# Kernel tuning notes

Hardware: AMD Instinct MI355X
Metric: run time of the kernel (lower is better)

Reference implementation:

```python
import jax, jax.numpy as jnp
import numpy as np

B, T, D, H, K, TAU, L = 1024, 168, 32, 512, 8, 24, 2


def _cell(Wih, Whh, bih, bhh, x_t, h, c):
    # PyTorch LSTM gate order: i, f, g, o
    gates = x_t @ Wih.T + bih + h @ Whh.T + bhh  # [B, 4H]
    i, f, g, o = jnp.split(gates, 4, axis=-1)
    c = jax.nn.sigmoid(f) * c + jax.nn.sigmoid(i) * jnp.tanh(g)
    h = jax.nn.sigmoid(o) * jnp.tanh(c)
    return h, c


def setup_inputs() -> dict:
    key = jax.random.key(0)
    ks = jax.random.split(key, 22)
    s = 1.0 / np.sqrt(H)

    def u(k, shape):
        return jax.random.uniform(k, shape, jnp.float32, -s, s)

    inp = {"x": jax.random.normal(ks[0], (B, T, D), jnp.float32)}
    # encoder LSTM (layer0 input D, layer1 input H)
    inp["enc_Wih0"] = u(ks[1], (4 * H, D)); inp["enc_Whh0"] = u(ks[2], (4 * H, H))
    inp["enc_bih0"] = u(ks[3], (4 * H,));  inp["enc_bhh0"] = u(ks[4], (4 * H,))
    inp["enc_Wih1"] = u(ks[5], (4 * H, H)); inp["enc_Whh1"] = u(ks[6], (4 * H, H))
    inp["enc_bih1"] = u(ks[7], (4 * H,));  inp["enc_bhh1"] = u(ks[8], (4 * H,))
    # decoder LSTM (both layers input H since d_enopt == d_model)
    inp["dec_Wih0"] = u(ks[9], (4 * H, H));  inp["dec_Whh0"] = u(ks[10], (4 * H, H))
    inp["dec_bih0"] = u(ks[11], (4 * H,));   inp["dec_bhh0"] = u(ks[12], (4 * H,))
    inp["dec_Wih1"] = u(ks[13], (4 * H, H)); inp["dec_Whh1"] = u(ks[14], (4 * H, H))
    inp["dec_bih1"] = u(ks[15], (4 * H,));   inp["dec_bhh1"] = u(ks[16], (4 * H,))
    # output heads
    inp["W1"] = u(ks[17], (K, H)); inp["b1"] = u(ks[18], (K,))
    inp["W2"] = u(ks[19], (K, H)); inp["b2"] = u(ks[20], (K,))
    return inp


def reference(x, enc_Wih0, enc_Whh0, enc_bih0, enc_bhh0,
              enc_Wih1, enc_Whh1, enc_bih1, enc_bhh1,
              dec_Wih0, dec_Whh0, dec_bih0, dec_bhh0,
              dec_Wih1, dec_Whh1, dec_bih1, dec_bhh1,
              W1, b1, W2, b2):
    enc_params = [(enc_Wih0, enc_Whh0, enc_bih0, enc_bhh0),
                  (enc_Wih1, enc_Whh1, enc_bih1, enc_bhh1)]
    dec_params = [(dec_Wih0, dec_Whh0, dec_bih0, dec_bhh0),
                  (dec_Wih1, dec_Whh1, dec_bih1, dec_bhh1)]
    b = x.shape[0]
    h0 = jnp.zeros((L, b, H), x.dtype)
    c0 = jnp.zeros((L, b, H), x.dtype)

    def enc_step(carry, x_t):
        h, c = carry
        inp = x_t
        hs, cs = [], []
        for l, p in enumerate(enc_params):
            hn, cn = _cell(*p, inp, h[l], c[l])
            hs.append(hn); cs.append(cn); inp = hn
        return (jnp.stack(hs), jnp.stack(cs)), None

    (h, c), _ = jax.lax.scan(enc_step, (h0, c0), jnp.swapaxes(x, 0, 1))

    def dec_step(carry, _):
        h, c = carry
        inp = h[L - 1]  # feed top-layer hidden back as input
        hs, cs = [], []
        for l, p in enumerate(dec_params):
            hn, cn = _cell(*p, inp, h[l], c[l])
            hs.append(hn); cs.append(cn); inp = hn
        return (jnp.stack(hs), jnp.stack(cs)), inp  # top-layer output

    _, outs = jax.lax.scan(dec_step, (h, c), None, length=TAU)  # [TAU, B, H]
    out = jnp.swapaxes(outs, 0, 1)  # [B, TAU, H]
    mu = out @ W1.T + b1
    beta = 2.0
    sigma = jax.nn.softplus(beta * (out @ W2.T + b2)) / beta
    return mu, sigma
```

## Files before the change

### kernel.cpp

```cpp
#include <hip/hip_runtime.h>
#include <math.h>

typedef _Float16 f16;
typedef __attribute__((ext_vector_type(8))) _Float16 f16x8;
typedef __attribute__((ext_vector_type(4))) _Float16 f16x4;
typedef __attribute__((ext_vector_type(4))) float f32x4;

namespace {
constexpr int B_ = 1024, T_ = 168, H_ = 512, K_ = 8, TAU_ = 24, U_ = 192;
}

__device__ __forceinline__ float sig_(float x) { return 1.0f / (1.0f + expf(-x)); }

template<int AUX>
__device__ __forceinline__ void gl16(const f16* g, char* l) {
    __builtin_amdgcn_global_load_lds((const __attribute__((address_space(1))) void*)g,
                                     (__attribute__((address_space(3))) void*)l, 16, 0, AUX);
}
__device__ __forceinline__ void st_h_sc1(f16* p, f16 v) {
    unsigned int u = (unsigned int)__builtin_bit_cast(unsigned short, v);
    asm volatile("global_store_short %0, %1, off sc1" :: "v"(p), "v"(u) : "memory");
}
#define MFMA16 __builtin_amdgcn_mfma_f32_16x16x32_f16

struct PP {
    const f16 *xp, *w0p, *wsW;
    const float* bsum;
    const f16* hzero;
    f16 *h0r, *h1r;
    f16* h1dec;
    int *cnt0, *cnt1;
};

extern "C" __global__ void __launch_bounds__(256, 2)
lstm_persist(PP P)
{
    extern __shared__ char lds[];
    const int tid = threadIdx.x;
    const int id2 = (blockIdx.x & 7) * 64 + (blockIdx.x >> 3);
    const int wv  = id2 & 63;
    const int chain = wv & 1;
    const int tt  = wv >> 1;
    const int rt  = tt & 15;
    const int jt  = (id2 >> 6) * 2 + (tt >> 4);
    const int row0 = rt * 64;
    const int j0   = jt * 32;

    const int lane = tid & 63, wid = tid >> 6;
    const int l16 = lane & 15, lq = lane >> 4;
    const int wr = wid >> 1, wc = wid & 1;
    const int sr = tid >> 3, sl = tid & 7;
    const long ksw = (long)((sl ^ (sr & 7)) << 3);

    auto wgf = [&](int q) {
        const int r = sr + 32 * q;
        return (long)(((r >> 4) & 3) * H_ + j0 + ((r >> 6) << 4) + (r & 15));
    };
    const long wgr0 = wgf(0), wgr1 = wgf(1), wgr2 = wgf(2), wgr3 = wgf(3);
    const long wgH0 = wgr0 * H_ + ksw, wgH1 = wgr1 * H_ + ksw;
    const long wgH2 = wgr2 * H_ + ksw, wgH3 = wgr3 * H_ + ksw;
    const long aH0k = (long)(row0 + sr) * H_ + ksw, aH1k = aH0k + 32 * H_;

    const int swz = (l16 & 7) << 4;
    const int ab0 = (wr * 32 + l16) * 128;
    const int ab1 = ab0 + 2048;
    const int wb0 = (wc * 64 + 0 * 16 + l16) * 128, wb1 = (wc * 64 + 1 * 16 + l16) * 128;
    const int wb2 = (wc * 64 + 2 * 16 + l16) * 128, wb3 = (wc * 64 + 3 * 16 + l16) * 128;

    const size_t WM  = (size_t)2048 * 512;
    const long   NBH = (long)B_ * H_;
    bool dead = false;

    auto waitf = [&](const int* p) {
        if (tid == 0 && !dead) {
            int tries = 0;
            while (__hip_atomic_load(p, __ATOMIC_RELAXED,
                                     __HIP_MEMORY_SCOPE_AGENT) < 16) {
                __builtin_amdgcn_s_sleep(1);
                if (++tries > (1 << 16)) { dead = true; break; }
            }
        }
        __syncthreads();
    };
    auto sig1 = [&](int* p) {
        asm volatile("s_waitcnt vmcnt(0)" ::: "memory");
        __syncthreads();
        if (tid == 0)
            __hip_atomic_fetch_add(p, 1, __ATOMIC_RELAXED, __HIP_MEMORY_SCOPE_AGENT);
    };

    auto computeChunk = [&](char* lb, f32x4 (&acc)[4][2]) {
        #pragma unroll
        for (int ks = 0; ks < 2; ++ks) {
            const int kb = ((ks * 64) + lq * 16) ^ swz;
            f16x8 ah0 = *(const f16x8*)(lb + ab0 + kb);
            f16x8 ah1 = *(const f16x8*)(lb + ab1 + kb);
            f16x8 w0 = *(const f16x8*)(lb + 8192 + wb0 + kb);
            f16x8 w1 = *(const f16x8*)(lb + 8192 + wb1 + kb);
            f16x8 w2 = *(const f16x8*)(lb + 8192 + wb2 + kb);
            f16x8 w3 = *(const f16x8*)(lb + 8192 + wb3 + kb);
            acc[0][0] = MFMA16(ah0, w0, acc[0][0], 0, 0, 0);
            acc[0][1] = MFMA16(ah1, w0, acc[0][1], 0, 0, 0);
            acc[1][0] = MFMA16(ah0, w1, acc[1][0], 0, 0, 0);
            acc[1][1] = MFMA16(ah1, w1, acc[1][1], 0, 0, 0);
            acc[2][0] = MFMA16(ah0, w2, acc[2][0], 0, 0, 0);
            acc[2][1] = MFMA16(ah1, w2, acc[2][1], 0, 0, 0);
            acc[3][0] = MFMA16(ah0, w3, acc[3][0], 0, 0, 0);
            acc[3][1] = MFMA16(ah1, w3, acc[3][1], 0, 0, 0);
        }
    };

    auto epiF = [&](const float* bg, float* cst, f16* hout, f32x4 (&a)[4][2]) {
        const int j = j0 + wc * 16 + l16;
        const float bg0 = bg[j], bg1 = bg[H_ + j];
        const float bg2 = bg[2 * H_ + j], bg3 = bg[3 * H_ + j];
        #pragma unroll
        for (int m = 0; m < 2; ++m)
            #pragma unroll
            for (int r = 0; r < 4; ++r) {
                const int ci = m * 4 + r;
                const int bb = row0 + wr * 32 + m * 16 + lq * 4 + r;
                const long base = (long)bb * H_ + j;
                const float pi = a[0][m][r] + bg0;
                const float pf = a[1][m][r] + bg1;
                const float pg = a[2][m][r] + bg2;
                const float po = a[3][m][r] + bg3;
                const float cn = sig_(pf) * cst[ci] + sig_(pi) * tanhf(pg);
                const float hn = sig_(po) * tanhf(cn);
                cst[ci] = cn;
                st_h_sc1(&hout[base], (f16)hn);
            }
    };

    float cst[8];
    #pragma unroll
    for (int i = 0; i < 8; ++i) cst[i] = 0.f;

    auto runCell = [&](const f16* Ain, long lda, int ncIn, long Kw,
                       const f16* Wih, const f16* Hin, const f16* Whh,
                       const float* bg, f16* hout) {
        const long aA0 = (long)(row0 + sr) * lda + ksw;
        const long aA1 = aA0 + 32 * lda;
        const long wK0 = wgr0 * Kw + ksw, wK1 = wgr1 * Kw + ksw;
        const long wK2 = wgr2 * Kw + ksw, wK3 = wgr3 * Kw + ksw;
        const int NC = ncIn + 8;
        auto st = [&](int ci) {
            char* lb = lds + (ci % 3) * 24576;
            const bool inp = ci < ncIn;
            const long k0 = (long)(inp ? ci : ci - ncIn) << 6;
            const f16* Ap = inp ? Ain : Hin;
            const f16* Wp = inp ? Wih : Whh;
            gl16<16>(Ap + (inp ? aA0 : aH0k) + k0, lb + tid * 16);
            gl16<16>(Ap + (inp ? aA1 : aH1k) + k0, lb + 4096 + tid * 16);
            gl16<0>(Wp + (inp ? wK0 : wgH0) + k0, lb + 8192  + tid * 16);
            gl16<0>(Wp + (inp ? wK1 : wgH1) + k0, lb + 12288 + tid * 16);
            gl16<0>(Wp + (inp ? wK2 : wgH2) + k0, lb + 16384 + tid * 16);
            gl16<0>(Wp + (inp ? wK3 : wgH3) + k0, lb + 20480 + tid * 16);
        };
        f32x4 acc[4][2];
        #pragma unroll
        for (int nf = 0; nf < 4; ++nf)
            #pragma unroll
            for (int m = 0; m < 2; ++m)
                #pragma unroll
                for (int q = 0; q < 4; ++q) acc[nf][m][q] = 0.f;
        st(0); st(1); st(2);
        for (int i = 0; i < NC; ++i) {
            const int ahead = (NC - 1 - i) < 2 ? (NC - 1 - i) : 2;
            if      (ahead == 2) asm volatile("s_waitcnt vmcnt(12)" ::: "memory");
            else if (ahead == 1) asm volatile("s_waitcnt vmcnt(6)"  ::: "memory");
            else                 asm volatile("s_waitcnt vmcnt(0)"  ::: "memory");
            __builtin_amdgcn_s_barrier();
            computeChunk(lds + (i % 3) * 24576, acc);
            asm volatile("s_waitcnt lgkmcnt(0)" ::: "memory");
            __builtin_amdgcn_s_barrier();
            if (i + 3 < NC) st(i + 3);
        }
        epiF(bg, cst, hout, acc);
    };

    if (chain == 0) {
        for (int u = 0; u < U_; ++u) {
            const bool dec = (u >= T_);
            if (u > 0) waitf(P.cnt0 + (u - 1) * 16 + rt);
            if (dec)   waitf(P.cnt1 + (u - 1) * 16 + rt);
            else if (u >= 8) waitf(P.cnt1 + (u - 8) * 16 + rt);
            const f16* h0prev = (u == 0) ? P.hzero : P.h0r + (long)((u - 1) & 7) * NBH;
            f16* h0out = P.h0r + (long)(u & 7) * NBH;
            if (dec) {
                const f16* h1prev = (u <= T_) ? P.h1r + (long)((u - 1) & 7) * NBH
                                              : P.h1dec + (long)(u - 1 - T_) * NBH;
                runCell(h1prev, H_, 8, H_, P.wsW + 3 * WM, h0prev,
                        P.wsW + 4 * WM, P.bsum + 4096, h0out);
            } else {
                runCell(P.xp + (long)u * B_ * 64, 64, 1, 64, P.w0p, h0prev,
                        P.wsW, P.bsum, h0out);
            }
            sig1(P.cnt0 + u * 16 + rt);
        }
    } else {
        for (int u = 0; u < U_; ++u) {
            const bool dec = (u >= T_);
            waitf(P.cnt0 + u * 16 + rt);
            if (u > 0) waitf(P.cnt1 + (u - 1) * 16 + rt);
            const f16* h1prev = (u == 0) ? P.hzero
                              : (u <= T_ ? P.h1r + (long)((u - 1) & 7) * NBH
                                         : P.h1dec + (long)(u - 1 - T_) * NBH);
            f16* h1out = (u < T_) ? P.h1r + (long)(u & 7) * NBH
                                  : P.h1dec + (long)(u - T_) * NBH;
            runCell(P.h0r + (long)(u & 7) * NBH, H_, 8, H_,
                    dec ? P.wsW + 5 * WM : P.wsW + 1 * WM, h1prev,
                    dec ? P.wsW + 6 * WM : P.wsW + 2 * WM,
                    P.bsum + (dec ? 6144 : 2048), h1out);
            sig1(P.cnt1 + u * 16 + rt);
        }
    }
}

extern "C" __global__ void __launch_bounds__(256)
padx_kernel(const float* __restrict__ x, f16* __restrict__ xp)
{
    const int idx = blockIdx.x * 256 + threadIdx.x;
    const int t = idx >> 10, b = idx & 1023;
    const float* src = x + ((long)b * T_ + t) * 32;
    f16* dst = xp + (long)idx * 64;
    #pragma unroll
    for (int q = 0; q < 8; ++q) {
        float4 v = *(const float4*)&src[q * 4];
        *(f16x4*)&dst[q * 4] = (f16x4){(f16)v.x, (f16)v.y, (f16)v.z, (f16)v.w};
    }
    #pragma unroll
    for (int q = 8; q < 16; ++q) *(f16x4*)&dst[q * 4] = (f16x4){0, 0, 0, 0};
}

extern "C" __global__ void __launch_bounds__(256)
padw_kernel(const float* __restrict__ w, f16* __restrict__ dst)
{
    const int idx = blockIdx.x * 256 + threadIdx.x;
    const int row = idx >> 4, k4 = idx & 15;
    f16x4 hv = (f16x4){0, 0, 0, 0};
    if (k4 < 8) {
        float4 v = *(const float4*)&w[(long)row * 32 + k4 * 4];
        hv = (f16x4){(f16)v.x, (f16)v.y, (f16)v.z, (f16)v.w};
    }
    *(f16x4*)&dst[(long)row * 64 + k4 * 4] = hv;
}

extern "C" __global__ void __launch_bounds__(256)
wcvt_kernel(const float* s0, const float* s1, const float* s2, const float* s3,
            const float* s4, const float* s5, const float* s6, f16* dst)
{
    const int i = blockIdx.x * 256 + threadIdx.x;
    if (i >= 7 * 262144) return;
    const int m = i >> 18, off = i & 262143;
    const float* s = m == 0 ? s0 : m == 1 ? s1 : m == 2 ? s2 : m == 3 ? s3
                   : m == 4 ? s4 : m == 5 ? s5 : s6;
    float4 v = ((const float4*)s)[off];
    *(f16x4*)&dst[(long)m * 1048576 + (long)off * 4] =
        (f16x4){(f16)v.x, (f16)v.y, (f16)v.z, (f16)v.w};
}

extern "C" __global__ void __launch_bounds__(256)
bias_kernel(const float* a0, const float* b0, const float* a1, const float* b1,
            const float* a2, const float* b2, const float* a3, const float* b3,
            float* out)
{
    const int i = blockIdx.x * 256 + threadIdx.x;
    const int l = i >> 11, k = i & 2047;
    const float* pa = l == 0 ? a0 : l == 1 ? a1 : l == 2 ? a2 : a3;
    const float* pb = l == 0 ? b0 : l == 1 ? b1 : l == 2 ? b2 : b3;
    out[i] = pa[k] + pb[k];
}

extern "C" __global__ void __launch_bounds__(256)
zero16(uint4* p, int n)
{
    for (int i = blockIdx.x * 256 + threadIdx.x; i < n; i += gridDim.x * 256)
        p[i] = make_uint4(0, 0, 0, 0);
}

extern "C" __global__ void __launch_bounds__(256)
head_all(const f16* __restrict__ h1dec,
         const float* __restrict__ W1, const float* __restrict__ b1,
         const float* __restrict__ W2, const float* __restrict__ b2,
         float* __restrict__ out)
{
    const int blk = blockIdx.x;
    const int s = blk >> 6;
    const int idx = (blk & 63) * 256 + threadIdx.x;
    const int b = idx >> 4, rr = idx & 15, k = rr & 7, which = rr >> 3;
    const float* w  = (which ? W2 : W1) + (long)k * H_;
    const f16*   hp = h1dec + ((long)s * B_ + b) * H_;
    float sum = 0.f;
    for (int d = 0; d < H_; d += 8) {
        f16x8  hv = *(const f16x8*)&hp[d];
        float4 w0 = *(const float4*)&w[d];
        float4 w1 = *(const float4*)&w[d + 4];
        sum = fmaf((float)hv[0], w0.x, sum);
        sum = fmaf((float)hv[1], w0.y, sum);
        sum = fmaf((float)hv[2], w0.z, sum);
        sum = fmaf((float)hv[3], w0.w, sum);
        sum = fmaf((float)hv[4], w1.x, sum);
        sum = fmaf((float)hv[5], w1.y, sum);
        sum = fmaf((float)hv[6], w1.z, sum);
        sum = fmaf((float)hv[7], w1.w, sum);
    }
    const long o = ((long)b * TAU_ + s) * K_ + k;
    if (which == 0) {
        out[o] = sum + b1[k];
    } else {
        float z  = 2.0f * (sum + b2[k]);
        float sp = fmaxf(z, 0.0f) + log1pf(expf(-fabsf(z)));
        out[(long)B_ * TAU_ * K_ + o] = 0.5f * sp;
    }
}

extern "C" void kernel_launch(void* const* d_in, const int* in_sizes, int n_in,
                              void* d_out, int out_size, void* d_ws, size_t ws_size,
                              hipStream_t stream)
{
    (void)in_sizes; (void)n_in; (void)out_size; (void)ws_size;

    const float* x     = (const float*)d_in[0];
    const float* eWih0 = (const float*)d_in[1];
    const float* eWhh0 = (const float*)d_in[2];
    const float* ebih0 = (const float*)d_in[3];
    const float* ebhh0 = (const float*)d_in[4];
    const float* eWih1 = (const float*)d_in[5];
    const float* eWhh1 = (const float*)d_in[6];
    const float* ebih1 = (const float*)d_in[7];
    const float* ebhh1 = (const float*)d_in[8];
    const float* dWih0 = (const float*)d_in[9];
    const float* dWhh0 = (const float*)d_in[10];
    const float* dbih0 = (const float*)d_in[11];
    const float* dbhh0 = (const float*)d_in[12];
    const float* dWih1 = (const float*)d_in[13];
    const float* dWhh1 = (const float*)d_in[14];
    const float* dbih1 = (const float*)d_in[15];
    const float* dbhh1 = (const float*)d_in[16];
    const float* W1    = (const float*)d_in[17];
    const float* b1    = (const float*)d_in[18];
    const float* W2    = (const float*)d_in[19];
    const float* b2    = (const float*)d_in[20];
    float* out = (float*)d_out;

    (void)hipFuncSetAttribute((const void*)lstm_persist,
                              hipFuncAttributeMaxDynamicSharedMemorySize, 73728);

    char* wsp = (char*)d_ws;
    auto take = [&](size_t n) { void* p = (void*)wsp; wsp += n; return p; };

    f16* xp    = (f16*)take((size_t)T_ * B_ * 64 * 2);
    f16* w0p   = (f16*)take((size_t)2048 * 64 * 2);
    f16* wsW   = (f16*)take((size_t)7 * 2048 * 512 * 2);
    float* bsum = (float*)take((size_t)4 * 2048 * 4);
    f16* h1dec = (f16*)take((size_t)TAU_ * B_ * H_ * 2);
    f16* h0r   = (f16*)take((size_t)8 * B_ * H_ * 2);
    f16* h1r   = (f16*)take((size_t)8 * B_ * H_ * 2);

    char* zstart = wsp;
    int* cnt0  = (int*)take((size_t)U_ * 16 * 4);
    int* cnt1  = (int*)take((size_t)U_ * 16 * 4);
    f16* hzero = (f16*)take((size_t)B_ * H_ * 2);
    const size_t zeroBytes = (size_t)(wsp - zstart);

    const dim3 blk(256);

    padx_kernel<<<dim3(T_ * B_ / 256), blk, 0, stream>>>(x, xp);
    padw_kernel<<<dim3(128), blk, 0, stream>>>(eWih0, w0p);
    wcvt_kernel<<<dim3(7168), blk, 0, stream>>>(eWhh0, eWih1, eWhh1, dWih0,
                                                dWhh0, dWih1, dWhh1, wsW);
    bias_kernel<<<dim3(32), blk, 0, stream>>>(ebih0, ebhh0, ebih1, ebhh1,
                                              dbih0, dbhh0, dbih1, dbhh1, bsum);
    zero16<<<dim3(256), blk, 0, stream>>>((uint4*)zstart, (int)(zeroBytes / 16));

    PP args;
    args.xp = xp; args.w0p = w0p; args.wsW = wsW; args.bsum = bsum; args.hzero = hzero;
    args.h0r = h0r; args.h1r = h1r; args.h1dec = h1dec;
    args.cnt0 = cnt0; args.cnt1 = cnt1;

    lstm_persist<<<dim3(512), blk, 73728, stream>>>(args);
    head_all<<<dim3(TAU_ * 64), blk, 0, stream>>>(h1dec, W1, b1, W2, b2, out);
}
```

Baseline: 6.114 ms.

## Merge both LSTM layer chains into one block with deeper 6-stage prefetch

Each persistent block now runs both layers for one tile instead of splitting layer 0 and layer 1 across separate blocks, which halves the grid to 256 blocks at one block per CU. The LDS ring grows from 3 to 6 stages, and chunk order is changed so the recurrent Whh/h chunks are loaded first. The input-projection chunks that depend on the other layer's output are gated by a mid-cell flag polled without blocking, so weight streaming overlaps the cross-block dependency wait. The trade-off is a serialised layer schedule within each block and the loss of two-blocks-per-CU occupancy.

```diff
diff --git a/kernel.cpp b/kernel.cpp
--- a/kernel.cpp
+++ b/kernel.cpp
@@ -32,19 +32,16 @@
     int *cnt0, *cnt1;
 };
 
-extern "C" __global__ void __launch_bounds__(256, 2)
+extern "C" __global__ void __launch_bounds__(256, 1)
 lstm_persist(PP P)
 {
     extern __shared__ char lds[];
+    int* flagSh = (int*)(lds + 6 * 24576);
     const int tid = threadIdx.x;
-    const int id2 = (blockIdx.x & 7) * 64 + (blockIdx.x >> 3);
-    const int wv  = id2 & 63;
-    const int chain = wv & 1;
-    const int tt  = wv >> 1;
-    const int rt  = tt & 15;
-    const int jt  = (id2 >> 6) * 2 + (tt >> 4);
+    const int id2 = (blockIdx.x & 7) * 32 + (blockIdx.x >> 3);
+    const int rt  = id2 & 15;
     const int row0 = rt * 64;
-    const int j0   = jt * 32;
+    const int j0   = (id2 >> 4) * 32;
 
     const int lane = tid & 63, wid = tid >> 6;
     const int l16 = lane & 15, lq = lane >> 4;
@@ -72,7 +69,7 @@
     bool dead = false;
 
     auto waitf = [&](const int* p) {
-        if (tid == 0 && !dead) {
+        if (tid == 0 && p && !dead) {
             int tries = 0;
             while (__hip_atomic_load(p, __ATOMIC_RELAXED,
                                      __HIP_MEMORY_SCOPE_AGENT) < 16) {
@@ -132,30 +129,30 @@
             }
     };
 
-    float cst[8];
+    float c0st[8], c1st[8];
     #pragma unroll
-    for (int i = 0; i < 8; ++i) cst[i] = 0.f;
+    for (int i = 0; i < 8; ++i) { c0st[i] = 0.f; c1st[i] = 0.f; }
 
     auto runCell = [&](const f16* Ain, long lda, int ncIn, long Kw,
                        const f16* Wih, const f16* Hin, const f16* Whh,
-                       const float* bg, f16* hout) {
+                       const float* bg, float* cst, f16* hout, const int* midFlag) {
         const long aA0 = (long)(row0 + sr) * lda + ksw;
         const long aA1 = aA0 + 32 * lda;
         const long wK0 = wgr0 * Kw + ksw, wK1 = wgr1 * Kw + ksw;
         const long wK2 = wgr2 * Kw + ksw, wK3 = wgr3 * Kw + ksw;
         const int NC = ncIn + 8;
-        auto st = [&](int ci) {
-            char* lb = lds + (ci % 3) * 24576;
-            const bool inp = ci < ncIn;
-            const long k0 = (long)(inp ? ci : ci - ncIn) << 6;
-            const f16* Ap = inp ? Ain : Hin;
-            const f16* Wp = inp ? Wih : Whh;
-            gl16<16>(Ap + (inp ? aA0 : aH0k) + k0, lb + tid * 16);
-            gl16<16>(Ap + (inp ? aA1 : aH1k) + k0, lb + 4096 + tid * 16);
-            gl16<0>(Wp + (inp ? wK0 : wgH0) + k0, lb + 8192  + tid * 16);
-            gl16<0>(Wp + (inp ? wK1 : wgH1) + k0, lb + 12288 + tid * 16);
-            gl16<0>(Wp + (inp ? wK2 : wgH2) + k0, lb + 16384 + tid * 16);
-            gl16<0>(Wp + (inp ? wK3 : wgH3) + k0, lb + 20480 + tid * 16);
+        auto st = [&](int g) {
+            char* lb = lds + (g % 6) * 24576;
+            const bool rc = g < 8;
+            const long k0 = (long)(rc ? g : g - 8) << 6;
+            const f16* Ap = rc ? Hin : Ain;
+            const f16* Wp = rc ? Whh : Wih;
+            gl16<16>(Ap + (rc ? aH0k : aA0) + k0, lb + tid * 16);
+            gl16<16>(Ap + (rc ? aH1k : aA1) + k0, lb + 4096 + tid * 16);
+            gl16<0>(Wp + (rc ? wgH0 : wK0) + k0, lb + 8192  + tid * 16);
+            gl16<0>(Wp + (rc ? wgH1 : wK1) + k0, lb + 12288 + tid * 16);
+            gl16<0>(Wp + (rc ? wgH2 : wK2) + k0, lb + 16384 + tid * 16);
+            gl16<0>(Wp + (rc ? wgH3 : wK3) + k0, lb + 20480 + tid * 16);
         };
         f32x4 acc[4][2];
         #pragma unroll
@@ -164,56 +161,67 @@
             for (int m = 0; m < 2; ++m)
                 #pragma unroll
                 for (int q = 0; q < 4; ++q) acc[nf][m][q] = 0.f;
-        st(0); st(1); st(2);
+
+        bool flagOK = (midFlag == nullptr);
+        int iss = 0;
+        while (iss < 5) { st(iss); ++iss; }
         for (int i = 0; i < NC; ++i) {
-            const int ahead = (NC - 1 - i) < 2 ? (NC - 1 - i) : 2;
-            if      (ahead == 2) asm volatile("s_waitcnt vmcnt(12)" ::: "memory");
-            else if (ahead == 1) asm volatile("s_waitcnt vmcnt(6)"  ::: "memory");
-            else                 asm volatile("s_waitcnt vmcnt(0)"  ::: "memory");
+            if (i >= iss) {
+                waitf(midFlag); flagOK = true;
+                st(iss); ++iss;
+            }
+            #pragma unroll 1
+            for (int b = 0; b < 2; ++b)
+                if (iss < NC && (iss - i) <= 5 && (flagOK || iss < 8)) { st(iss); ++iss; }
+            if (!flagOK && tid == 0)
+                *flagSh = (__hip_atomic_load(midFlag, __ATOMIC_RELAXED,
+                                             __HIP_MEMORY_SCOPE_AGENT) >= 16) ? 1 : 0;
+            const int k = (iss - i - 1) > 5 ? 5 : (iss - i - 1);
+            switch (k) {
+                case 5: asm volatile("s_waitcnt vmcnt(30)" ::: "memory"); break;
+                case 4: asm volatile("s_waitcnt vmcnt(24)" ::: "memory"); break;
+                case 3: asm volatile("s_waitcnt vmcnt(18)" ::: "memory"); break;
+                case 2: asm volatile("s_waitcnt vmcnt(12)" ::: "memory"); break;
+                case 1: asm volatile("s_waitcnt vmcnt(6)"  ::: "memory"); break;
+                default: asm volatile("s_waitcnt vmcnt(0)" ::: "memory"); break;
+            }
             __builtin_amdgcn_s_barrier();
-            computeChunk(lds + (i % 3) * 24576, acc);
+            if (!flagOK) flagOK = (*flagSh != 0);
+            computeChunk(lds + (i % 6) * 24576, acc);
             asm volatile("s_waitcnt lgkmcnt(0)" ::: "memory");
             __builtin_amdgcn_s_barrier();
-            if (i + 3 < NC) st(i + 3);
         }
         epiF(bg, cst, hout, acc);
     };
 
-    if (chain == 0) {
-        for (int u = 0; u < U_; ++u) {
-            const bool dec = (u >= T_);
-            if (u > 0) waitf(P.cnt0 + (u - 1) * 16 + rt);
-            if (dec)   waitf(P.cnt1 + (u - 1) * 16 + rt);
-            else if (u >= 8) waitf(P.cnt1 + (u - 8) * 16 + rt);
-            const f16* h0prev = (u == 0) ? P.hzero : P.h0r + (long)((u - 1) & 7) * NBH;
-            f16* h0out = P.h0r + (long)(u & 7) * NBH;
-            if (dec) {
-                const f16* h1prev = (u <= T_) ? P.h1r + (long)((u - 1) & 7) * NBH
-                                              : P.h1dec + (long)(u - 1 - T_) * NBH;
-                runCell(h1prev, H_, 8, H_, P.wsW + 3 * WM, h0prev,
-                        P.wsW + 4 * WM, P.bsum + 4096, h0out);
-            } else {
-                runCell(P.xp + (long)u * B_ * 64, 64, 1, 64, P.w0p, h0prev,
-                        P.wsW, P.bsum, h0out);
-            }
-            sig1(P.cnt0 + u * 16 + rt);
+    for (int u = 0; u < U_; ++u) {
+        const bool dec = (u >= T_);
+        const f16* h0prev = (u == 0) ? P.hzero : P.h0r + (long)((u - 1) & 7) * NBH;
+        const f16* h1prev = (u == 0) ? P.hzero
+                          : (u <= T_ ? P.h1r + (long)((u - 1) & 7) * NBH
+                                     : P.h1dec + (long)(u - 1 - T_) * NBH);
+        f16* h0out = P.h0r + (long)(u & 7) * NBH;
+
+        if (u > 0) waitf(P.cnt0 + (u - 1) * 16 + rt);
+        if (dec) {
+            runCell(h1prev, H_, 8, H_, P.wsW + 3 * WM, h0prev,
+                    P.wsW + 4 * WM, P.bsum + 4096, c0st, h0out,
+                    P.cnt1 + (u - 1) * 16 + rt);
+        } else {
+            runCell(P.xp + (long)u * B_ * 64, 64, 1, 64, P.w0p, h0prev,
+                    P.wsW, P.bsum, c0st, h0out, nullptr);
         }
-    } else {
-        for (int u = 0; u < U_; ++u) {
-            const bool dec = (u >= T_);
-            waitf(P.cnt0 + u * 16 + rt);
-            if (u > 0) waitf(P.cnt1 + (u - 1) * 16 + rt);
-            const f16* h1prev = (u == 0) ? P.hzero
-                              : (u <= T_ ? P.h1r + (long)((u - 1) & 7) * NBH
-                                         : P.h1dec + (long)(u - 1 - T_) * NBH);
-            f16* h1out = (u < T_) ? P.h1r + (long)(u & 7) * NBH
-                                  : P.h1dec + (long)(u - T_) * NBH;
-            runCell(P.h0r + (long)(u & 7) * NBH, H_, 8, H_,
-                    dec ? P.wsW + 5 * WM : P.wsW + 1 * WM, h1prev,
-                    dec ? P.wsW + 6 * WM : P.wsW + 2 * WM,
-                    P.bsum + (dec ? 6144 : 2048), h1out);
-            sig1(P.cnt1 + u * 16 + rt);
-        }
+        sig1(P.cnt0 + u * 16 + rt);
+
+        if (u > 0) waitf(P.cnt1 + (u - 1) * 16 + rt);
+        f16* h1out = (u < T_) ? P.h1r + (long)(u & 7) * NBH
+                              : P.h1dec + (long)(u - T_) * NBH;
+        runCell(h0out, H_, 8, H_,
+                dec ? P.wsW + 5 * WM : P.wsW + 1 * WM, h1prev,
+                dec ? P.wsW + 6 * WM : P.wsW + 2 * WM,
+                P.bsum + (dec ? 6144 : 2048), c1st, h1out,
+                P.cnt0 + u * 16 + rt);
+        sig1(P.cnt1 + u * 16 + rt);
     }
 }
 
@@ -345,7 +353,7 @@
     float* out = (float*)d_out;
 
     (void)hipFuncSetAttribute((const void*)lstm_persist,
-                              hipFuncAttributeMaxDynamicSharedMemorySize, 73728);
+                              hipFuncAttributeMaxDynamicSharedMemorySize, 147472);
 
     char* wsp = (char*)d_ws;
     auto take = [&](size_t n) { void* p = (void*)wsp; wsp += n; return p; };
@@ -379,6 +387,6 @@
     args.h0r = h0r; args.h1r = h1r; args.h1dec = h1dec;
     args.cnt0 = cnt0; args.cnt1 = cnt1;
 
-    lstm_persist<<<dim3(512), blk, 73728, stream>>>(args);
+    lstm_persist<<<dim3(256), blk, 147472, stream>>>(args);
     head_all<<<dim3(TAU_ * 64), blk, 0, stream>>>(h1dec, W1, b1, W2, b2, out);
 }
```

New measurement: 5.153 ms. -15.7%, faster.
